# Performance work log

Hardware: AMD Instinct MI355X
Metric: run time of the kernel (lower is better)

Reference implementation:

```python
import jax, jax.numpy as jnp
import numpy as np

NUM_HEADS = 8
LN_EPS = 1e-5


def _comm_matrix(E):
    # chain graph: connection (i, i+1) with weight 0.5, symmetric
    cm = jnp.zeros((E, E), dtype=jnp.float32)
    idx = jnp.arange(E - 1)
    cm = cm.at[idx, idx + 1].set(0.5)
    return cm + cm.T


def setup_inputs() -> dict:
    key = jax.random.key(0)
    B, E, H = 2048, 16, 1024
    ks = jax.random.split(key, 8)
    s = 0.02
    return {
        "x": jax.random.normal(ks[0], (B, E, H), dtype=jnp.float32),
        "ln_g": jnp.ones((H,), jnp.float32),
        "ln_b": jnp.zeros((H,), jnp.float32),
        "wq": jax.random.normal(ks[1], (H, H), jnp.float32) * s,
        "bq": jnp.zeros((H,), jnp.float32),
        "wk": jax.random.normal(ks[2], (H, H), jnp.float32) * s,
        "bk": jnp.zeros((H,), jnp.float32),
        "wv": jax.random.normal(ks[3], (H, H), jnp.float32) * s,
        "bv": jnp.zeros((H,), jnp.float32),
        "wo": jax.random.normal(ks[4], (H, H), jnp.float32) * s,
        "bo": jnp.zeros((H,), jnp.float32),
        "wg": jax.random.normal(ks[5], (1, 2 * H), jnp.float32) * s,
        "bg": jnp.zeros((1,), jnp.float32),
    }


def reference(x, ln_g, ln_b, wq, bq, wk, bk, wv, bv, wo, bo, wg, bg):
    B, E, H = x.shape
    nh = NUM_HEADS
    hd = H // nh

    # --- graph communication: comm_matrix @ x over expert dim ---
    cm = _comm_matrix(E)                              # [E, E]
    comm = jnp.einsum('ef,bfh->beh', cm, x)           # [B, E, H]

    # --- cross-attention block (pre-LN, residual) ---
    residual = comm
    mu = comm.mean(-1, keepdims=True)
    var = comm.var(-1, keepdims=True)
    xn = (comm - mu) * jax.lax.rsqrt(var + LN_EPS) * ln_g + ln_b

    q = (xn @ wq.T + bq).reshape(B, E, nh, hd)
    k = (xn @ wk.T + bk).reshape(B, E, nh, hd)
    v = (xn @ wv.T + bv).reshape(B, E, nh, hd)

    scores = jnp.einsum('bqnd,bknd->bnqk', q, k) / (hd ** 0.5)  # [B, nh, E, E]
    attn = jax.nn.softmax(scores, axis=-1)
    attended = jnp.einsum('bnqk,bknd->bqnd', attn, v).reshape(B, E, H)
    comm_out = attended @ wo.T + bo + residual        # [B, E, H]

    # --- communication gate ---
    gate_in = jnp.concatenate([x, comm_out], axis=-1)  # [B, E, 2H]
    gate = jax.nn.sigmoid(gate_in @ wg.T + bg)         # [B, E, 1]
    return gate * comm_out + (1.0 - gate) * x
```

## Files before the change

### kernel.cpp

```cpp
#include <hip/hip_runtime.h>
#include <cstdint>
#include <cstddef>

#define HDIM 1024
#define EEXP 16
#define BATCH 2048
#define MROWS (BATCH * EEXP)
#define NHEADS 8
#define HEADD 128
#define KDIM 1024
#define LN_EPS 1e-5f

typedef __bf16 bf16x8_t __attribute__((ext_vector_type(8)));
typedef float f32x4_t __attribute__((ext_vector_type(4)));
typedef int i32x4_t __attribute__((ext_vector_type(4)));
typedef unsigned short u16x4_t __attribute__((ext_vector_type(4)));
typedef unsigned short u16x8_t __attribute__((ext_vector_type(8)));

__device__ __forceinline__ unsigned short f2bf(float f) {
    unsigned int u = __builtin_bit_cast(unsigned int, f);
    unsigned int r = (u + 0x7FFFu + ((u >> 16) & 1u)) >> 16;
    return (unsigned short)r;
}
__device__ __forceinline__ float bf2f(unsigned short h) {
    unsigned int u = ((unsigned int)h) << 16;
    return __builtin_bit_cast(float, u);
}

__global__ __launch_bounds__(256) void k_conv4(
    const float* __restrict__ s0, const float* __restrict__ s1,
    const float* __restrict__ s2, const float* __restrict__ s3,
    unsigned short* __restrict__ d0, unsigned short* __restrict__ d1,
    unsigned short* __restrict__ d2, unsigned short* __restrict__ d3) {
    const int which = blockIdx.x >> 10;
    const int i = ((blockIdx.x & 1023) * 256 + threadIdx.x) * 4;
    const float* s = (which == 0) ? s0 : (which == 1) ? s1 : (which == 2) ? s2 : s3;
    unsigned short* d = (which == 0) ? d0 : (which == 1) ? d1 : (which == 2) ? d2 : d3;
    float4 v = *(const float4*)(s + i);
    u16x4_t o;
    o.x = f2bf(v.x); o.y = f2bf(v.y); o.z = f2bf(v.z); o.w = f2bf(v.w);
    *(u16x4_t*)(d + i) = o;
}

__global__ __launch_bounds__(256) void k_prep(const float* __restrict__ x,
                                              const float* __restrict__ lng,
                                              const float* __restrict__ lnb,
                                              unsigned short* __restrict__ xn) {
    const int m = blockIdx.x;
    const int e = m & (EEXP - 1);
    const int t = threadIdx.x;
    const int h = t * 4;
    const float* xr = x + (size_t)m * HDIM;

    float c0 = 0.f, c1 = 0.f, c2 = 0.f, c3 = 0.f;
    if (e > 0) {
        float4 v = *(const float4*)(xr - HDIM + h);
        c0 = 0.5f * v.x; c1 = 0.5f * v.y; c2 = 0.5f * v.z; c3 = 0.5f * v.w;
    }
    if (e < EEXP - 1) {
        float4 v = *(const float4*)(xr + HDIM + h);
        c0 += 0.5f * v.x; c1 += 0.5f * v.y; c2 += 0.5f * v.z; c3 += 0.5f * v.w;
    }
    float s  = c0 + c1 + c2 + c3;
    float ss = c0 * c0 + c1 * c1 + c2 * c2 + c3 * c3;
#pragma unroll
    for (int off = 32; off; off >>= 1) {
        s  += __shfl_xor(s, off, 64);
        ss += __shfl_xor(ss, off, 64);
    }
    __shared__ float red[8];
    const int wv = t >> 6;
    if ((t & 63) == 0) { red[wv] = s; red[4 + wv] = ss; }
    __syncthreads();
    s  = red[0] + red[1] + red[2] + red[3];
    ss = red[4] + red[5] + red[6] + red[7];
    const float mean = s * (1.0f / HDIM);
    const float var  = ss * (1.0f / HDIM) - mean * mean;
    const float rinv = rsqrtf(var + LN_EPS);

    float4 g = *(const float4*)(lng + h);
    float4 b = *(const float4*)(lnb + h);
    u16x4_t o;
    o.x = f2bf((c0 - mean) * rinv * g.x + b.x);
    o.y = f2bf((c1 - mean) * rinv * g.y + b.y);
    o.z = f2bf((c2 - mean) * rinv * g.z + b.z);
    o.w = f2bf((c3 - mean) * rinv * g.w + b.w);
    *(u16x4_t*)(xn + (size_t)m * HDIM + h) = o;
}

template <int N, bool IS_QKV>
__global__ __launch_bounds__(512, 2) void k_gemm2(
    const unsigned short* __restrict__ A,
    const unsigned short* __restrict__ Bw,
    const float* __restrict__ b0,
    const float* __restrict__ b1,
    const float* __restrict__ b2,
    unsigned short* __restrict__ Cbf,
    float* __restrict__ Cf) {
    constexpr int K = KDIM;
    __shared__ unsigned short S[65536];

    const int tid  = threadIdx.x;
    const int lane = tid & 63;
    const int wave = tid >> 6;
    const int quad = lane >> 4, r16 = lane & 15;
    const int wm2  = wave >> 2, wn4 = wave & 3;

    const int xcd = blockIdx.x & 7;
    const int g   = blockIdx.x >> 3;
    int mt, nt;
    if constexpr (N == 3072) {
        const int st = g / 48, r = g % 48;
        mt = xcd * 16 + st * 4 + (r & 3);
        nt = r >> 2;
    } else {
        const int st = g >> 4, r = g & 15;
        mt = xcd * 16 + st * 4 + (r & 3);
        nt = r >> 2;
    }
    const int m0 = mt * 256, n0 = nt * 256;

    const int srow0 = tid >> 3;
    const int gk = ((tid & 7) ^ (srow0 & 7)) * 8;
    const unsigned short* Ag = A  + (size_t)(m0 + srow0) * K + gk;
    const unsigned short* Bg = Bw + (size_t)(n0 + srow0) * K + gk;

    const int swz0 = ((0 + quad) ^ (r16 & 7)) * 8;
    const int swz1 = ((4 + quad) ^ (r16 & 7)) * 8;
    const int aBase = wm2 * 8192 + r16 * 64;
    const int bBase = (2 + (wn4 >> 1)) * 8192 + (wn4 & 1) * 4096 + r16 * 64;

    const int aA_0_0 = 2 * (aBase + swz0);
    const int aA_0_1 = 2 * (aBase + swz1);
    const int aA_1_0 = aA_0_0 + 65536;
    const int aA_1_1 = aA_0_1 + 65536;
    const int bA_0_0 = 2 * (bBase + swz0);
    const int bA_0_1 = 2 * (bBase + swz1);
    const int bA_1_0 = bA_0_0 + 65536;
    const int bA_1_1 = bA_0_1 + 65536;

    f32x4_t acc[8][4];
#pragma unroll
    for (int f = 0; f < 8; ++f)
#pragma unroll
        for (int j = 0; j < 4; ++j) acc[f][j] = f32x4_t{0.f, 0.f, 0.f, 0.f};

    i32x4_t bq0_0, bq0_1, bq1_0, bq1_1, bq2_0, bq2_1, bq3_0, bq3_1;

#define DSR(dst, addr, imm) \
    asm volatile("ds_read_b128 %0, %1 offset:%2" : "=v"(dst) : "v"(addr), "n"(imm))

#define BF(x) __builtin_bit_cast(bf16x8_t, x)

#define STG(reg, srcb, rowoff, kk0)                                                          \
    do {                                                                                     \
        __builtin_amdgcn_global_load_lds(                                                    \
            (const __attribute__((address_space(1))) void*)((srcb) + (size_t)(rowoff) * K + (kk0)),       \
            (__attribute__((address_space(3))) void*)(S + (reg) * 8192 + tid * 8), 16, 0, 0);             \
        __builtin_amdgcn_global_load_lds(                                                    \
            (const __attribute__((address_space(1))) void*)((srcb) + (size_t)((rowoff) + 64) * K + (kk0)),\
            (__attribute__((address_space(3))) void*)(S + (reg) * 8192 + 4096 + tid * 8), 16, 0, 0);      \
    } while (0)

#define DSRD_B(buf)                                                                          \
    do {                                                                                     \
        DSR(bq0_0, bA_##buf##_0, 0 * 2048); DSR(bq0_1, bA_##buf##_1, 0 * 2048);              \
        DSR(bq1_0, bA_##buf##_0, 1 * 2048); DSR(bq1_1, bA_##buf##_1, 1 * 2048);              \
        DSR(bq2_0, bA_##buf##_0, 2 * 2048); DSR(bq2_1, bA_##buf##_1, 2 * 2048);              \
        DSR(bq3_0, bA_##buf##_0, 3 * 2048); DSR(bq3_1, bA_##buf##_1, 3 * 2048);              \
    } while (0)

#define VM4 asm volatile("s_waitcnt vmcnt(4)" ::: "memory")
#define VM0 asm volatile("s_waitcnt vmcnt(0)" ::: "memory")
#define NOSTG ((void)0)
#define NOWAIT ((void)0)

#define MMJ(ph, s2, ar0, ar1)                                                                \
    acc[(ph)*2+(s2)][0] = __builtin_amdgcn_mfma_f32_16x16x32_bf16(BF(bq0_0), BF(ar0), acc[(ph)*2+(s2)][0], 0, 0, 0); \
    acc[(ph)*2+(s2)][0] = __builtin_amdgcn_mfma_f32_16x16x32_bf16(BF(bq0_1), BF(ar1), acc[(ph)*2+(s2)][0], 0, 0, 0); \
    acc[(ph)*2+(s2)][1] = __builtin_amdgcn_mfma_f32_16x16x32_bf16(BF(bq1_0), BF(ar0), acc[(ph)*2+(s2)][1], 0, 0, 0); \
    acc[(ph)*2+(s2)][1] = __builtin_amdgcn_mfma_f32_16x16x32_bf16(BF(bq1_1), BF(ar1), acc[(ph)*2+(s2)][1], 0, 0, 0); \
    acc[(ph)*2+(s2)][2] = __builtin_amdgcn_mfma_f32_16x16x32_bf16(BF(bq2_0), BF(ar0), acc[(ph)*2+(s2)][2], 0, 0, 0); \
    acc[(ph)*2+(s2)][2] = __builtin_amdgcn_mfma_f32_16x16x32_bf16(BF(bq2_1), BF(ar1), acc[(ph)*2+(s2)][2], 0, 0, 0); \
    acc[(ph)*2+(s2)][3] = __builtin_amdgcn_mfma_f32_16x16x32_bf16(BF(bq3_0), BF(ar0), acc[(ph)*2+(s2)][3], 0, 0, 0); \
    acc[(ph)*2+(s2)][3] = __builtin_amdgcn_mfma_f32_16x16x32_bf16(BF(bq3_1), BF(ar1), acc[(ph)*2+(s2)][3], 0, 0, 0);

#define PHASE(buf, ph, STAGE_STMT, WAIT_STMT)                                                \
    do {                                                                                     \
        i32x4_t a0_0, a0_1, a1_0, a1_1;                                                      \
        DSR(a0_0, aA_##buf##_0, ((ph) * 2 + 0) * 2048);                                      \
        DSR(a0_1, aA_##buf##_1, ((ph) * 2 + 0) * 2048);                                      \
        DSR(a1_0, aA_##buf##_0, ((ph) * 2 + 1) * 2048);                                      \
        DSR(a1_1, aA_##buf##_1, ((ph) * 2 + 1) * 2048);                                      \
        STAGE_STMT;                                                                          \
        __builtin_amdgcn_s_barrier();                                                        \
        asm volatile("s_waitcnt lgkmcnt(0)" ::: "memory");                                   \
        __builtin_amdgcn_sched_barrier(0);                                                   \
        __builtin_amdgcn_s_setprio(1);                                                       \
        MMJ(ph, 0, a0_0, a0_1)                                                               \
        MMJ(ph, 1, a1_0, a1_1)                                                               \
        __builtin_amdgcn_s_setprio(0);                                                       \
        __builtin_amdgcn_sched_barrier(0);                                                   \
        WAIT_STMT;                                                                           \
        __builtin_amdgcn_s_barrier();                                                        \
    } while (0)

    STG(0, Ag, 0,   0);
    STG(1, Ag, 128, 0);
    STG(2, Bg, 0,   0);
    STG(3, Bg, 128, 0);
    STG(6, Bg, 0,   64);
    STG(7, Bg, 128, 64);
    VM4;
    __builtin_amdgcn_s_barrier();

#pragma unroll 1
    for (int i = 0; i < 7; ++i) {
        const int kA1 = (2 * i + 1) * 64;
        const int kN2 = (2 * i + 2) * 64;
        const int kN3 = (2 * i + 3) * 64;
        DSRD_B(0);
        PHASE(0, 0, STG(4, Ag, 0,   kA1), NOWAIT);
        PHASE(0, 1, STG(5, Ag, 128, kA1), NOWAIT);
        PHASE(0, 2, STG(2, Bg, 0,   kN2), NOWAIT);
        PHASE(0, 3, STG(3, Bg, 128, kN2), VM4);
        DSRD_B(1);
        PHASE(1, 0, STG(0, Ag, 0,   kN2), NOWAIT);
        PHASE(1, 1, STG(1, Ag, 128, kN2), NOWAIT);
        PHASE(1, 2, STG(6, Bg, 0,   kN3), NOWAIT);
        PHASE(1, 3, STG(7, Bg, 128, kN3), VM4);
    }
    {
        DSRD_B(0);
        PHASE(0, 0, STG(4, Ag, 0,   960), NOWAIT);
        PHASE(0, 1, STG(5, Ag, 128, 960), NOWAIT);
        PHASE(0, 2, NOSTG, NOWAIT);
        PHASE(0, 3, NOSTG, VM0);
        DSRD_B(1);
        PHASE(1, 0, NOSTG, NOWAIT);
        PHASE(1, 1, NOSTG, NOWAIT);
        PHASE(1, 2, NOSTG, NOWAIT);
        PHASE(1, 3, NOSTG, NOWAIT);
    }

    f32x4_t bias4[4];
#pragma unroll
    for (int j = 0; j < 4; ++j) {
        const int gcol = n0 + wn4 * 64 + j * 16 + quad * 4;
        const float* bp;
        if constexpr (IS_QKV) {
            bp = (gcol < 1024) ? (b0 + gcol)
               : (gcol < 2048) ? (b1 + gcol - 1024)
                               : (b2 + gcol - 2048);
        } else {
            bp = b0 + gcol;
        }
        bias4[j] = *(const f32x4_t*)bp;
    }

#pragma unroll
    for (int f = 0; f < 8; ++f) {
        const int grow = m0 + wm2 * 128 + f * 16 + r16;
#pragma unroll
        for (int j = 0; j < 4; ++j) {
            const int gcol = n0 + wn4 * 64 + j * 16 + quad * 4;
            if constexpr (IS_QKV) {
                u16x4_t o;
                o.x = f2bf(acc[f][j][0] + bias4[j][0]);
                o.y = f2bf(acc[f][j][1] + bias4[j][1]);
                o.z = f2bf(acc[f][j][2] + bias4[j][2]);
                o.w = f2bf(acc[f][j][3] + bias4[j][3]);
                *(u16x4_t*)&Cbf[(size_t)grow * N + gcol] = o;
            } else {
                f32x4_t o;
                o[0] = acc[f][j][0] + bias4[j][0];
                o[1] = acc[f][j][1] + bias4[j][1];
                o[2] = acc[f][j][2] + bias4[j][2];
                o[3] = acc[f][j][3] + bias4[j][3];
                *(f32x4_t*)&Cf[(size_t)grow * N + gcol] = o;
            }
        }
    }
#undef DSR
#undef BF
#undef STG
#undef DSRD_B
#undef PHASE
#undef MMJ
#undef VM4
#undef VM0
#undef NOSTG
#undef NOWAIT
}

__global__ __launch_bounds__(256) void k_attn(const unsigned short* __restrict__ qkv,
                                              unsigned short* __restrict__ att) {
    const int bidx = blockIdx.x;
    const int b = bidx >> 3, n = bidx & 7;
    __shared__ float qs[16][132], ks[16][132], vs[16][132];
    __shared__ float ps[16][17];
    const int t = threadIdx.x;

    {
        const int row = t >> 4, c0 = (t & 15) * 8;
        const size_t base = (size_t)(b * EEXP + row) * (3 * HDIM) + n * HEADD + c0;
        u16x8_t qv = *(const u16x8_t*)&qkv[base];
        u16x8_t kv = *(const u16x8_t*)&qkv[base + HDIM];
        u16x8_t vv = *(const u16x8_t*)&qkv[base + 2 * HDIM];
        f32x4_t q0, q1, k0, k1, v0, v1;
#pragma unroll
        for (int u = 0; u < 4; u++) {
            q0[u] = bf2f(qv[u]); q1[u] = bf2f(qv[u + 4]);
            k0[u] = bf2f(kv[u]); k1[u] = bf2f(kv[u + 4]);
            v0[u] = bf2f(vv[u]); v1[u] = bf2f(vv[u + 4]);
        }
        *(f32x4_t*)&qs[row][c0] = q0; *(f32x4_t*)&qs[row][c0 + 4] = q1;
        *(f32x4_t*)&ks[row][c0] = k0; *(f32x4_t*)&ks[row][c0 + 4] = k1;
        *(f32x4_t*)&vs[row][c0] = v0; *(f32x4_t*)&vs[row][c0 + 4] = v1;
    }
    __syncthreads();

    const int qe = t >> 4, ke = t & 15;
    float s = 0.f;
#pragma unroll
    for (int d = 0; d < HEADD; d += 4) {
        f32x4_t qv = *(const f32x4_t*)&qs[qe][d];
        f32x4_t kv = *(const f32x4_t*)&ks[ke][d];
        s += qv[0] * kv[0] + qv[1] * kv[1] + qv[2] * kv[2] + qv[3] * kv[3];
    }
    s *= 0.08838834764831845f;
    float mx = s;
#pragma unroll
    for (int off = 8; off; off >>= 1) mx = fmaxf(mx, __shfl_xor(mx, off, 16));
    const float ex = __expf(s - mx);
    float sum = ex;
#pragma unroll
    for (int off = 8; off; off >>= 1) sum += __shfl_xor(sum, off, 16);
    ps[qe][ke] = ex / sum;
    __syncthreads();

    const int dd8 = (t & 15) * 8;
    float o[8] = {0.f, 0.f, 0.f, 0.f, 0.f, 0.f, 0.f, 0.f};
#pragma unroll
    for (int k2 = 0; k2 < EEXP; k2++) {
        const float p = ps[qe][k2];
        f32x4_t v0 = *(const f32x4_t*)&vs[k2][dd8];
        f32x4_t v1 = *(const f32x4_t*)&vs[k2][dd8 + 4];
        o[0] += p * v0[0]; o[1] += p * v0[1]; o[2] += p * v0[2]; o[3] += p * v0[3];
        o[4] += p * v1[0]; o[5] += p * v1[1]; o[6] += p * v1[2]; o[7] += p * v1[3];
    }
    u16x8_t ov;
#pragma unroll
    for (int u = 0; u < 8; u++) ov[u] = f2bf(o[u]);
    *(u16x8_t*)&att[(size_t)(b * EEXP + qe) * HDIM + n * HEADD + dd8] = ov;
}

__global__ __launch_bounds__(256) void k_gate(const float* __restrict__ x,
                                              const float* __restrict__ wg,
                                              const float* __restrict__ bg,
                                              float* __restrict__ out) {
    const int m = blockIdx.x;
    const int e = m & (EEXP - 1);
    const int t = threadIdx.x;
    const int h = t * 4;
    const float* xr = x + (size_t)m * HDIM;
    float* orow = out + (size_t)m * HDIM;

    float4 xv = *(const float4*)(xr + h);
    float4 rv = *(const float4*)(orow + h);
    float c0 = 0.f, c1 = 0.f, c2 = 0.f, c3 = 0.f;
    if (e > 0) {
        float4 v = *(const float4*)(xr - HDIM + h);
        c0 = 0.5f * v.x; c1 = 0.5f * v.y; c2 = 0.5f * v.z; c3 = 0.5f * v.w;
    }
    if (e < EEXP - 1) {
        float4 v = *(const float4*)(xr + HDIM + h);
        c0 += 0.5f * v.x; c1 += 0.5f * v.y; c2 += 0.5f * v.z; c3 += 0.5f * v.w;
    }
    const float co0 = rv.x + c0, co1 = rv.y + c1, co2 = rv.z + c2, co3 = rv.w + c3;

    float4 w1 = *(const float4*)(wg + h);
    float4 w2 = *(const float4*)(wg + HDIM + h);
    float d = xv.x * w1.x + xv.y * w1.y + xv.z * w1.z + xv.w * w1.w +
              co0 * w2.x + co1 * w2.y + co2 * w2.z + co3 * w2.w;
#pragma unroll
    for (int off = 32; off; off >>= 1) d += __shfl_xor(d, off, 64);
    __shared__ float red[4];
    const int wv = t >> 6;
    if ((t & 63) == 0) red[wv] = d;
    __syncthreads();
    const float tot = red[0] + red[1] + red[2] + red[3] + bg[0];
    const float gate = 1.0f / (1.0f + __expf(-tot));

    float4 ov;
    ov.x = gate * co0 + (1.0f - gate) * xv.x;
    ov.y = gate * co1 + (1.0f - gate) * xv.y;
    ov.z = gate * co2 + (1.0f - gate) * xv.z;
    ov.w = gate * co3 + (1.0f - gate) * xv.w;
    *(float4*)(orow + h) = ov;
}

extern "C" void kernel_launch(void* const* d_in, const int* in_sizes, int n_in,
                              void* d_out, int out_size, void* d_ws, size_t ws_size,
                              hipStream_t stream) {
    const float* x   = (const float*)d_in[0];
    const float* lng = (const float*)d_in[1];
    const float* lnb = (const float*)d_in[2];
    const float* wq  = (const float*)d_in[3];
    const float* bq  = (const float*)d_in[4];
    const float* wk  = (const float*)d_in[5];
    const float* bk  = (const float*)d_in[6];
    const float* wv  = (const float*)d_in[7];
    const float* bv  = (const float*)d_in[8];
    const float* wo  = (const float*)d_in[9];
    const float* bo  = (const float*)d_in[10];
    const float* wg  = (const float*)d_in[11];
    const float* bg  = (const float*)d_in[12];
    float* out = (float*)d_out;

    unsigned short* wqkv = (unsigned short*)d_ws;
    unsigned short* wob  = wqkv + (size_t)3072 * 1024;
    unsigned short* xn   = wob + (size_t)1024 * 1024;
    unsigned short* qkv  = xn + (size_t)MROWS * HDIM;
    unsigned short* att  = qkv + (size_t)MROWS * 3 * HDIM;

    const int WELTS = 1024 * 1024;
    k_conv4<<<4096, 256, 0, stream>>>(wq, wk, wv, wo,
                                      wqkv, wqkv + (size_t)WELTS,
                                      wqkv + (size_t)2 * WELTS, wob);

    k_prep<<<MROWS, 256, 0, stream>>>(x, lng, lnb, xn);

    k_gemm2<3072, true><<<(MROWS / 256) * (3072 / 256), 512, 0, stream>>>(
        xn, wqkv, bq, bk, bv, qkv, nullptr);

    k_attn<<<BATCH * NHEADS, 256, 0, stream>>>(qkv, att);

    k_gemm2<1024, false><<<(MROWS / 256) * (1024 / 256), 512, 0, stream>>>(
        att, wob, bo, nullptr, nullptr, nullptr, out);

    k_gate<<<MROWS, 256, 0, stream>>>(x, wg, bg, out);
}
```

Baseline: 713.8 us.

## Software-pipeline LDS fragment reads with double-buffered registers in GEMM main loop

Restructures the GEMM inner loop so that LDS reads for the next phase's A fragments and the next buffer's B fragments are issued before the current phase's MFMAs. Waits use partial lgkmcnt counts instead of draining all LDS reads before each MFMA block. The point is to hide LDS latency behind matrix math. The cost is roughly double the fragment registers, which can raise VGPR pressure, and vmcnt waits now drain fully to 0 instead of 4.

Result: no change. 725.2 us (+1.6%).

```diff
diff --git a/kernel.cpp b/kernel.cpp
--- a/kernel.cpp
+++ b/kernel.cpp
@@ -145,12 +145,29 @@
 #pragma unroll
         for (int j = 0; j < 4; ++j) acc[f][j] = f32x4_t{0.f, 0.f, 0.f, 0.f};
 
-    i32x4_t bq0_0, bq0_1, bq1_0, bq1_1, bq2_0, bq2_1, bq3_0, bq3_1;
+    i32x4_t pA0, pA1, pA2, pA3;
+    i32x4_t qA0, qA1, qA2, qA3;
+    i32x4_t bX00, bX01, bX10, bX11, bX20, bX21, bX30, bX31;
+    i32x4_t bY00, bY01, bY10, bY11, bY20, bY21, bY30, bY31;
 
 #define DSR(dst, addr, imm) \
     asm volatile("ds_read_b128 %0, %1 offset:%2" : "=v"(dst) : "v"(addr), "n"(imm))
-
 #define BF(x) __builtin_bit_cast(bf16x8_t, x)
+#define MF(b, a, c) __builtin_amdgcn_mfma_f32_16x16x32_bf16(BF(b), BF(a), (c), 0, 0, 0)
+
+#define RD_A(SET, abuf, fb)                                \
+    do {                                                   \
+        DSR(SET##0, aA_##abuf##_0, (fb) * 2048);           \
+        DSR(SET##1, aA_##abuf##_1, (fb) * 2048);           \
+        DSR(SET##2, aA_##abuf##_0, ((fb) + 1) * 2048);     \
+        DSR(SET##3, aA_##abuf##_1, ((fb) + 1) * 2048);     \
+    } while (0)
+
+#define RD_B2(SB, bbuf, j)                                 \
+    do {                                                   \
+        DSR(b##SB##j##0, bA_##bbuf##_0, (j) * 2048);       \
+        DSR(b##SB##j##1, bA_##bbuf##_1, (j) * 2048);       \
+    } while (0)
 
 #define STG(reg, srcb, rowoff, kk0)                                                          \
     do {                                                                                     \
@@ -162,47 +179,39 @@
             (__attribute__((address_space(3))) void*)(S + (reg) * 8192 + 4096 + tid * 8), 16, 0, 0);      \
     } while (0)
 
-#define DSRD_B(buf)                                                                          \
-    do {                                                                                     \
-        DSR(bq0_0, bA_##buf##_0, 0 * 2048); DSR(bq0_1, bA_##buf##_1, 0 * 2048);              \
-        DSR(bq1_0, bA_##buf##_0, 1 * 2048); DSR(bq1_1, bA_##buf##_1, 1 * 2048);              \
-        DSR(bq2_0, bA_##buf##_0, 2 * 2048); DSR(bq2_1, bA_##buf##_1, 2 * 2048);              \
-        DSR(bq3_0, bA_##buf##_0, 3 * 2048); DSR(bq3_1, bA_##buf##_1, 3 * 2048);              \
-    } while (0)
-
-#define VM4 asm volatile("s_waitcnt vmcnt(4)" ::: "memory")
-#define VM0 asm volatile("s_waitcnt vmcnt(0)" ::: "memory")
-#define NOSTG ((void)0)
-#define NOWAIT ((void)0)
-
-#define MMJ(ph, s2, ar0, ar1)                                                                \
-    acc[(ph)*2+(s2)][0] = __builtin_amdgcn_mfma_f32_16x16x32_bf16(BF(bq0_0), BF(ar0), acc[(ph)*2+(s2)][0], 0, 0, 0); \
-    acc[(ph)*2+(s2)][0] = __builtin_amdgcn_mfma_f32_16x16x32_bf16(BF(bq0_1), BF(ar1), acc[(ph)*2+(s2)][0], 0, 0, 0); \
-    acc[(ph)*2+(s2)][1] = __builtin_amdgcn_mfma_f32_16x16x32_bf16(BF(bq1_0), BF(ar0), acc[(ph)*2+(s2)][1], 0, 0, 0); \
-    acc[(ph)*2+(s2)][1] = __builtin_amdgcn_mfma_f32_16x16x32_bf16(BF(bq1_1), BF(ar1), acc[(ph)*2+(s2)][1], 0, 0, 0); \
-    acc[(ph)*2+(s2)][2] = __builtin_amdgcn_mfma_f32_16x16x32_bf16(BF(bq2_0), BF(ar0), acc[(ph)*2+(s2)][2], 0, 0, 0); \
-    acc[(ph)*2+(s2)][2] = __builtin_amdgcn_mfma_f32_16x16x32_bf16(BF(bq2_1), BF(ar1), acc[(ph)*2+(s2)][2], 0, 0, 0); \
-    acc[(ph)*2+(s2)][3] = __builtin_amdgcn_mfma_f32_16x16x32_bf16(BF(bq3_0), BF(ar0), acc[(ph)*2+(s2)][3], 0, 0, 0); \
-    acc[(ph)*2+(s2)][3] = __builtin_amdgcn_mfma_f32_16x16x32_bf16(BF(bq3_1), BF(ar1), acc[(ph)*2+(s2)][3], 0, 0, 0);
-
-#define PHASE(buf, ph, STAGE_STMT, WAIT_STMT)                                                \
-    do {                                                                                     \
-        i32x4_t a0_0, a0_1, a1_0, a1_1;                                                      \
-        DSR(a0_0, aA_##buf##_0, ((ph) * 2 + 0) * 2048);                                      \
-        DSR(a0_1, aA_##buf##_1, ((ph) * 2 + 0) * 2048);                                      \
-        DSR(a1_0, aA_##buf##_0, ((ph) * 2 + 1) * 2048);                                      \
-        DSR(a1_1, aA_##buf##_1, ((ph) * 2 + 1) * 2048);                                      \
-        STAGE_STMT;                                                                          \
-        __builtin_amdgcn_s_barrier();                                                        \
-        asm volatile("s_waitcnt lgkmcnt(0)" ::: "memory");                                   \
-        __builtin_amdgcn_sched_barrier(0);                                                   \
-        __builtin_amdgcn_s_setprio(1);                                                       \
-        MMJ(ph, 0, a0_0, a0_1)                                                               \
-        MMJ(ph, 1, a1_0, a1_1)                                                               \
-        __builtin_amdgcn_s_setprio(0);                                                       \
-        __builtin_amdgcn_sched_barrier(0);                                                   \
-        WAIT_STMT;                                                                           \
-        __builtin_amdgcn_s_barrier();                                                        \
+#define LGKM(n) asm volatile("s_waitcnt lgkmcnt(" #n ")")
+#define VMW asm volatile("s_waitcnt vmcnt(0)" ::: "memory")
+#define NOVM ((void)0)
+
+#define MMPH(fa, AS, BS)                                         \
+    acc[(fa)][0]   = MF(b##BS##00, AS##0, acc[(fa)][0]);         \
+    acc[(fa)][0]   = MF(b##BS##01, AS##1, acc[(fa)][0]);         \
+    acc[(fa)][1]   = MF(b##BS##10, AS##0, acc[(fa)][1]);         \
+    acc[(fa)][1]   = MF(b##BS##11, AS##1, acc[(fa)][1]);         \
+    acc[(fa)][2]   = MF(b##BS##20, AS##0, acc[(fa)][2]);         \
+    acc[(fa)][2]   = MF(b##BS##21, AS##1, acc[(fa)][2]);         \
+    acc[(fa)][3]   = MF(b##BS##30, AS##0, acc[(fa)][3]);         \
+    acc[(fa)][3]   = MF(b##BS##31, AS##1, acc[(fa)][3]);         \
+    acc[(fa)+1][0] = MF(b##BS##00, AS##2, acc[(fa)+1][0]);       \
+    acc[(fa)+1][0] = MF(b##BS##01, AS##3, acc[(fa)+1][0]);       \
+    acc[(fa)+1][1] = MF(b##BS##10, AS##2, acc[(fa)+1][1]);       \
+    acc[(fa)+1][1] = MF(b##BS##11, AS##3, acc[(fa)+1][1]);       \
+    acc[(fa)+1][2] = MF(b##BS##20, AS##2, acc[(fa)+1][2]);       \
+    acc[(fa)+1][2] = MF(b##BS##21, AS##3, acc[(fa)+1][2]);       \
+    acc[(fa)+1][3] = MF(b##BS##30, AS##2, acc[(fa)+1][3]);       \
+    acc[(fa)+1][3] = MF(b##BS##31, AS##3, acc[(fa)+1][3]);
+
+#define CORE(lgN, fa, AS, BS, VMSTMT)                 \
+    do {                                              \
+        __builtin_amdgcn_s_barrier();                 \
+        LGKM(lgN);                                    \
+        __builtin_amdgcn_sched_barrier(0);            \
+        __builtin_amdgcn_s_setprio(1);                \
+        MMPH(fa, AS, BS)                              \
+        __builtin_amdgcn_s_setprio(0);                \
+        __builtin_amdgcn_sched_barrier(0);            \
+        VMSTMT;                                       \
+        __builtin_amdgcn_s_barrier();                 \
     } while (0)
 
     STG(0, Ag, 0,   0);
@@ -211,36 +220,58 @@
     STG(3, Bg, 128, 0);
     STG(6, Bg, 0,   64);
     STG(7, Bg, 128, 64);
-    VM4;
+    VMW;
     __builtin_amdgcn_s_barrier();
+    RD_B2(X, 0, 0); RD_B2(X, 0, 1); RD_B2(X, 0, 2); RD_B2(X, 0, 3);
 
 #pragma unroll 1
     for (int i = 0; i < 7; ++i) {
         const int kA1 = (2 * i + 1) * 64;
         const int kN2 = (2 * i + 2) * 64;
         const int kN3 = (2 * i + 3) * 64;
-        DSRD_B(0);
-        PHASE(0, 0, STG(4, Ag, 0,   kA1), NOWAIT);
-        PHASE(0, 1, STG(5, Ag, 128, kA1), NOWAIT);
-        PHASE(0, 2, STG(2, Bg, 0,   kN2), NOWAIT);
-        PHASE(0, 3, STG(3, Bg, 128, kN2), VM4);
-        DSRD_B(1);
-        PHASE(1, 0, STG(0, Ag, 0,   kN2), NOWAIT);
-        PHASE(1, 1, STG(1, Ag, 128, kN2), NOWAIT);
-        PHASE(1, 2, STG(6, Bg, 0,   kN3), NOWAIT);
-        PHASE(1, 3, STG(7, Bg, 128, kN3), VM4);
+        RD_A(pA, 0, 0); RD_A(qA, 0, 2); RD_B2(Y, 1, 0);
+        STG(4, Ag, 0, kA1);
+        CORE(6, 0, pA, X, NOVM);
+        RD_A(pA, 0, 4); RD_B2(Y, 1, 1);
+        STG(5, Ag, 128, kA1);
+        CORE(8, 2, qA, X, NOVM);
+        RD_A(qA, 0, 6); RD_B2(Y, 1, 2);
+        STG(2, Bg, 0, kN2);
+        CORE(8, 4, pA, X, NOVM);
+        RD_B2(Y, 1, 3);
+        STG(3, Bg, 128, kN2);
+        CORE(4, 6, qA, X, VMW);
+        RD_A(pA, 1, 0); RD_A(qA, 1, 2); RD_B2(X, 0, 0);
+        STG(0, Ag, 0, kN2);
+        CORE(6, 0, pA, Y, NOVM);
+        RD_A(pA, 1, 4); RD_B2(X, 0, 1);
+        STG(1, Ag, 128, kN2);
+        CORE(8, 2, qA, Y, NOVM);
+        RD_A(qA, 1, 6); RD_B2(X, 0, 2);
+        STG(6, Bg, 0, kN3);
+        CORE(8, 4, pA, Y, NOVM);
+        RD_B2(X, 0, 3);
+        STG(7, Bg, 128, kN3);
+        CORE(4, 6, qA, Y, VMW);
     }
     {
-        DSRD_B(0);
-        PHASE(0, 0, STG(4, Ag, 0,   960), NOWAIT);
-        PHASE(0, 1, STG(5, Ag, 128, 960), NOWAIT);
-        PHASE(0, 2, NOSTG, NOWAIT);
-        PHASE(0, 3, NOSTG, VM0);
-        DSRD_B(1);
-        PHASE(1, 0, NOSTG, NOWAIT);
-        PHASE(1, 1, NOSTG, NOWAIT);
-        PHASE(1, 2, NOSTG, NOWAIT);
-        PHASE(1, 3, NOSTG, NOWAIT);
+        RD_A(pA, 0, 0); RD_A(qA, 0, 2); RD_B2(Y, 1, 0);
+        STG(4, Ag, 0, 960);
+        CORE(6, 0, pA, X, NOVM);
+        RD_A(pA, 0, 4); RD_B2(Y, 1, 1);
+        STG(5, Ag, 128, 960);
+        CORE(8, 2, qA, X, NOVM);
+        RD_A(qA, 0, 6); RD_B2(Y, 1, 2);
+        CORE(8, 4, pA, X, NOVM);
+        RD_B2(Y, 1, 3);
+        CORE(4, 6, qA, X, VMW);
+        RD_A(pA, 1, 0); RD_A(qA, 1, 2);
+        CORE(4, 0, pA, Y, NOVM);
+        RD_A(pA, 1, 4);
+        CORE(4, 2, qA, Y, NOVM);
+        RD_A(qA, 1, 6);
+        CORE(4, 4, pA, Y, NOVM);
+        CORE(0, 6, qA, Y, NOVM);
     }
 
     f32x4_t bias4[4];
@@ -283,14 +314,15 @@
     }
 #undef DSR
 #undef BF
+#undef MF
+#undef RD_A
+#undef RD_B2
 #undef STG
-#undef DSRD_B
-#undef PHASE
-#undef MMJ
-#undef VM4
-#undef VM0
-#undef NOSTG
-#undef NOWAIT
+#undef LGKM
+#undef VMW
+#undef NOVM
+#undef MMPH
+#undef CORE
 }
 
 __global__ __launch_bounds__(256) void k_attn(const unsigned short* __restrict__ qkv,
```
